# Kernel tuning notes

Measured on AMD Instinct MI355X. Metric: run time of the kernel, lower is better.

The kernel has to match this reference:

```python
import jax, jax.numpy as jnp
import numpy as np

HIDDEN = 4096
NUM_HEADS = 32
NUM_KV_HEADS = 8
HEAD_DIM = 128
EPS = 1e-6
ROPE_THETA = 1000000.0
T = 2048


def setup_inputs() -> dict:
    key = jax.random.key(0)
    k1, k2, k3, k4, k5 = jax.random.split(key, 5)
    q_size = NUM_HEADS * HEAD_DIM
    kv_size = NUM_KV_HEADS * HEAD_DIM
    return {
        "positions": jnp.arange(T, dtype=jnp.int32),
        "hidden_states": jax.random.normal(k1, (T, HIDDEN), dtype=jnp.float32),
        "w_qkv": jax.random.normal(k2, (HIDDEN, q_size + 2 * kv_size), dtype=jnp.float32) * 0.02,
        "w_o": jax.random.normal(k3, (q_size, HIDDEN), dtype=jnp.float32) * 0.02,
        "q_norm_w": jnp.ones((HEAD_DIM,), dtype=jnp.float32) + 0.01 * jax.random.normal(k4, (HEAD_DIM,), dtype=jnp.float32),
        "k_norm_w": jnp.ones((HEAD_DIM,), dtype=jnp.float32) + 0.01 * jax.random.normal(k5, (HEAD_DIM,), dtype=jnp.float32),
    }


def _rms_norm(x, w, eps=EPS):
    # x: [..., head_dim], normalize over last dim
    var = jnp.mean(jnp.square(x), axis=-1, keepdims=True)
    return x * jax.lax.rsqrt(var + eps) * w


def _apply_rope(x, positions):
    # neox-style rotate-half RoPE, rotary_dim == head_dim
    d = x.shape[-1]
    inv_freq = 1.0 / (ROPE_THETA ** (jnp.arange(0, d, 2, dtype=jnp.float32) / d))
    freqs = positions.astype(jnp.float32)[:, None] * inv_freq[None, :]  # [T, d/2]
    cos = jnp.cos(freqs)[:, None, :]  # [T, 1, d/2]
    sin = jnp.sin(freqs)[:, None, :]
    x1, x2 = jnp.split(x, 2, axis=-1)
    return jnp.concatenate([x1 * cos - x2 * sin, x2 * cos + x1 * sin], axis=-1)


def reference(positions, hidden_states, w_qkv, w_o, q_norm_w, k_norm_w):
    num_tokens = hidden_states.shape[0]
    q_size = NUM_HEADS * HEAD_DIM
    kv_size = NUM_KV_HEADS * HEAD_DIM
    group = NUM_HEADS // NUM_KV_HEADS

    qkv = hidden_states @ w_qkv  # [T, q+2kv]
    q = qkv[:, :q_size].reshape(num_tokens, NUM_HEADS, HEAD_DIM)
    k = qkv[:, q_size:q_size + kv_size].reshape(num_tokens, NUM_KV_HEADS, HEAD_DIM)
    v = qkv[:, q_size + kv_size:].reshape(num_tokens, NUM_KV_HEADS, HEAD_DIM)

    q = _rms_norm(q, q_norm_w)
    k = _rms_norm(k, k_norm_w)
    q = _apply_rope(q, positions)
    k = _apply_rope(k, positions)

    scale = HEAD_DIM ** -0.5
    # GQA: group query heads over shared kv heads
    qg = q.reshape(num_tokens, NUM_KV_HEADS, group, HEAD_DIM)
    scores = jnp.einsum("tkgd,skd->kgts", qg * scale, k)  # [KH, G, T, S]
    causal = positions[:, None] >= positions[None, :]  # [T, S]
    scores = jnp.where(causal[None, None, :, :], scores, jnp.finfo(scores.dtype).min)
    probs = jax.nn.softmax(scores, axis=-1)
    out = jnp.einsum("kgts,skd->tkgd", probs, v)  # [T, KH, G, D]
    out = out.reshape(num_tokens, q_size)
    return out @ w_o
```

## Files before the change

kernel.cpp:

```cpp
#include <hip/hip_runtime.h>
#include <cstdint>
#include <cstddef>

#define T_TOK 2048
#define HID   4096
#define NQH   32
#define NKVH  8
#define HD    128
#define QKV_N 6144

typedef __bf16 bf16x8 __attribute__((ext_vector_type(8)));
typedef __bf16 bf16x4 __attribute__((ext_vector_type(4)));
typedef float  f32x4  __attribute__((ext_vector_type(4)));
typedef float  f32x16 __attribute__((ext_vector_type(16)));

#define AS1 __attribute__((address_space(1)))
#define AS3 __attribute__((address_space(3)))

__device__ __forceinline__ void gll16(const void* g, void* l) {
  __builtin_amdgcn_global_load_lds((const AS1 void*)g, (AS3 void*)l, 16, 0, 0);
}

__global__ __launch_bounds__(256) void k_convert(const float* __restrict__ in,
                                                 __bf16* __restrict__ out, int n4) {
  int i = blockIdx.x * 256 + threadIdx.x;
  if (i >= n4) return;
  float4 v = ((const float4*)in)[i];
  bf16x4 o;
  o[0] = (__bf16)v.x; o[1] = (__bf16)v.y; o[2] = (__bf16)v.z; o[3] = (__bf16)v.w;
  ((bf16x4*)out)[i] = o;
}

__global__ __launch_bounds__(256) void k_transpose(const float* __restrict__ in,
                                                   __bf16* __restrict__ out,
                                                   int R, int C) {
  __shared__ float tile[64][33];
  const int tid = threadIdx.x;
  const int c0 = blockIdx.x * 32, r0 = blockIdx.y * 64;
  const int ty = tid >> 3, tx = tid & 7;
#pragma unroll
  for (int k = 0; k < 2; ++k) {
    float4 v = *(const float4*)&in[(size_t)(r0 + ty + k * 32) * C + c0 + tx * 4];
    tile[ty + k * 32][tx * 4 + 0] = v.x;
    tile[ty + k * 32][tx * 4 + 1] = v.y;
    tile[ty + k * 32][tx * 4 + 2] = v.z;
    tile[ty + k * 32][tx * 4 + 3] = v.w;
  }
  __syncthreads();
  const int c = tid >> 3, rq = tid & 7;
  bf16x8 o;
#pragma unroll
  for (int i = 0; i < 8; ++i) o[i] = (__bf16)tile[rq * 8 + i][c];
  *(bf16x8*)&out[(size_t)(c0 + c) * R + r0 + rq * 8] = o;
}

__global__ __launch_bounds__(256) void k_vtrans(const float* __restrict__ qkv,
                                                __bf16* __restrict__ vt) {
  __shared__ float tile[64][33];
  const int tid = threadIdx.x;
  const int kvh = blockIdx.z;
  const int d0 = blockIdx.x * 32;
  const int t0 = blockIdx.y * 64;
  const int ty = tid >> 3, tx = tid & 7;
#pragma unroll
  for (int k = 0; k < 2; ++k) {
    float4 v = *(const float4*)&qkv[(size_t)(t0 + ty + k * 32) * QKV_N + 5120 + kvh * 128 + d0 + tx * 4];
    tile[ty + k * 32][tx * 4 + 0] = v.x;
    tile[ty + k * 32][tx * 4 + 1] = v.y;
    tile[ty + k * 32][tx * 4 + 2] = v.z;
    tile[ty + k * 32][tx * 4 + 3] = v.w;
  }
  __syncthreads();
  const int d = tid >> 3, tq = tid & 7;
  bf16x8 o;
#pragma unroll
  for (int i = 0; i < 8; ++i) o[i] = (__bf16)tile[tq * 8 + i][d];
  *(bf16x8*)&vt[((size_t)kvh * 128 + d0 + d) * T_TOK + t0 + tq * 8] = o;
}

template <int NFR>
__global__ __launch_bounds__(512, 2) void k_gemm8(const __bf16* __restrict__ A,
                                                  const __bf16* __restrict__ Bt,
                                                  float* __restrict__ C,
                                                  int N, int K) {
  constexpr int BN   = 64 * NFR;
  constexpr int WN   = 16 * NFR;
  constexpr int NB   = NFR / 2;
  constexpr int NH   = NFR / 2;
  constexpr int BREG = BN * 64;
  constexpr int BUFSZ = 16384 + 2 * BREG;
  __shared__ alignas(16) char ldsb[2 * BUFSZ];
  const int tid = threadIdx.x;
  const int lane = tid & 63, w = tid >> 6;
  const int l16 = lane & 15, lg = lane >> 4;
  const int wm = w >> 2, wn = w & 3;

  const int x = blockIdx.x & 7, idx = blockIdx.x >> 3;
  const int bm = (x & 1) * 8 + (idx & 7);
  const int bn = (x >> 1) * 4 + (idx >> 3);

  const int rA = tid >> 2, pA = tid & 3;
  const __bf16* asrc = A + (size_t)(bm * 128 + rA) * K + ((pA ^ ((rA >> 1) & 3)) * 8);
  const __bf16* bsrc = Bt + (size_t)(bn * BN + rA) * K + ((pA ^ ((rA >> 1) & 3)) * 8);

#define RA_(buf, mk) (ldsb + (buf) * BUFSZ + (mk) * 8192)
#define RB_(buf, mk) (ldsb + (buf) * BUFSZ + 16384 + (mk) * BREG)
#define STG_A(buf, mk, kk) { gll16(asrc + (kk) + (mk) * 32, RA_(buf, mk) + w * 1024); }
#define STG_B(buf, mk, kk) { _Pragma("unroll") \
    for (int j = 0; j < NB; ++j) \
      gll16(bsrc + (size_t)j * 128 * K + (kk) + (mk) * 32, RB_(buf, mk) + j * 8192 + w * 1024); }
#define FRAG(base, row) (*(const bf16x8*)((base) + (row) * 64 + ((lg ^ (((row) >> 1) & 3)) << 4)))
#define WAITN() { if constexpr (NFR == 6) asm volatile("s_waitcnt vmcnt(4)" ::: "memory"); \
                  else                    asm volatile("s_waitcnt vmcnt(3)" ::: "memory"); }

  f32x4 acc[4][NFR] = {};
  const int nkt = K >> 6;

  STG_A(0, 0, 0); STG_B(0, 0, 0); STG_A(0, 1, 0); STG_B(0, 1, 0);

  for (int t = 0; t < nkt - 1; ++t) {
    const int cur = t & 1, nxt = cur ^ 1;
    const int kn = (t + 1) * 64;
    bf16x8 af[4], bf_[NH];

    STG_A(nxt, 0, kn);
    WAITN();
    __builtin_amdgcn_s_barrier();
    __builtin_amdgcn_sched_barrier(0);
#pragma unroll
    for (int i = 0; i < 4; ++i) af[i] = FRAG(RA_(cur, 0), wm * 64 + i * 16 + l16);
#pragma unroll
    for (int n = 0; n < NH; ++n) bf_[n] = FRAG(RB_(cur, 0), wn * WN + n * 16 + l16);
    __builtin_amdgcn_s_setprio(1);
#pragma unroll
    for (int i = 0; i < 4; ++i)
#pragma unroll
      for (int n = 0; n < NH; ++n)
        acc[i][n] = __builtin_amdgcn_mfma_f32_16x16x32_bf16(af[i], bf_[n], acc[i][n], 0, 0, 0);
    __builtin_amdgcn_s_setprio(0);
    __builtin_amdgcn_s_barrier();

#pragma unroll
    for (int n = 0; n < NH; ++n) bf_[n] = FRAG(RB_(cur, 0), wn * WN + (NH + n) * 16 + l16);
    STG_B(nxt, 0, kn);
    __builtin_amdgcn_s_barrier();
    __builtin_amdgcn_s_setprio(1);
#pragma unroll
    for (int i = 0; i < 4; ++i)
#pragma unroll
      for (int n = 0; n < NH; ++n)
        acc[i][NH + n] = __builtin_amdgcn_mfma_f32_16x16x32_bf16(af[i], bf_[n], acc[i][NH + n], 0, 0, 0);
    __builtin_amdgcn_s_setprio(0);
    __builtin_amdgcn_s_barrier();

    STG_A(nxt, 1, kn);
    WAITN();
    __builtin_amdgcn_s_barrier();
    __builtin_amdgcn_sched_barrier(0);
#pragma unroll
    for (int i = 0; i < 4; ++i) af[i] = FRAG(RA_(cur, 1), wm * 64 + i * 16 + l16);
#pragma unroll
    for (int n = 0; n < NH; ++n) bf_[n] = FRAG(RB_(cur, 1), wn * WN + n * 16 + l16);
    __builtin_amdgcn_s_setprio(1);
#pragma unroll
    for (int i = 0; i < 4; ++i)
#pragma unroll
      for (int n = 0; n < NH; ++n)
        acc[i][n] = __builtin_amdgcn_mfma_f32_16x16x32_bf16(af[i], bf_[n], acc[i][n], 0, 0, 0);
    __builtin_amdgcn_s_setprio(0);
    __builtin_amdgcn_s_barrier();

#pragma unroll
    for (int n = 0; n < NH; ++n) bf_[n] = FRAG(RB_(cur, 1), wn * WN + (NH + n) * 16 + l16);
    STG_B(nxt, 1, kn);
    __builtin_amdgcn_s_barrier();
    __builtin_amdgcn_s_setprio(1);
#pragma unroll
    for (int i = 0; i < 4; ++i)
#pragma unroll
      for (int n = 0; n < NH; ++n)
        acc[i][NH + n] = __builtin_amdgcn_mfma_f32_16x16x32_bf16(af[i], bf_[n], acc[i][NH + n], 0, 0, 0);
    __builtin_amdgcn_s_setprio(0);
    __builtin_amdgcn_s_barrier();
  }

  asm volatile("s_waitcnt vmcnt(0)" ::: "memory");
  __builtin_amdgcn_s_barrier();
  __builtin_amdgcn_sched_barrier(0);
  {
    const int cur = (nkt - 1) & 1;
#pragma unroll
    for (int mk = 0; mk < 2; ++mk) {
      bf16x8 aa[4], bb[NFR];
#pragma unroll
      for (int i = 0; i < 4; ++i) aa[i] = FRAG(RA_(cur, mk), wm * 64 + i * 16 + l16);
#pragma unroll
      for (int n = 0; n < NFR; ++n) bb[n] = FRAG(RB_(cur, mk), wn * WN + n * 16 + l16);
#pragma unroll
      for (int i = 0; i < 4; ++i)
#pragma unroll
        for (int n = 0; n < NFR; ++n)
          acc[i][n] = __builtin_amdgcn_mfma_f32_16x16x32_bf16(aa[i], bb[n], acc[i][n], 0, 0, 0);
    }
  }
#undef RA_
#undef RB_
#undef STG_A
#undef STG_B
#undef FRAG
#undef WAITN

#pragma unroll
  for (int mi = 0; mi < 4; ++mi)
#pragma unroll
    for (int ni = 0; ni < NFR; ++ni) {
      int row = bm * 128 + wm * 64 + mi * 16 + lg * 4;
      int col = bn * BN + wn * WN + ni * 16 + l16;
#pragma unroll
      for (int r = 0; r < 4; ++r)
        C[(size_t)(row + r) * N + col] = acc[mi][ni][r];
    }
}

__global__ __launch_bounds__(256) void k_norm_rope(const float* __restrict__ qkv,
                                                   const int* __restrict__ pos,
                                                   const float* __restrict__ qw,
                                                   const float* __restrict__ kw,
                                                   __bf16* __restrict__ qo,
                                                   __bf16* __restrict__ ko) {
  const int t = blockIdx.x;
  const int w = threadIdx.x >> 6, i = threadIdx.x & 63;
  const float fr = (float)pos[t] * expf((float)i * -0.21586735246819178f);
  const float cs = cosf(fr), sn = sinf(fr);
  const float qwi1 = qw[i], qwi2 = qw[i + 64];
  const float kwi1 = kw[i], kwi2 = kw[i + 64];
  const float* base = qkv + (size_t)t * QKV_N;
#pragma unroll
  for (int s = 0; s < 10; ++s) {
    const int slot = w * 10 + s;
    const int off = (slot < 32) ? slot * 128 : 4096 + (slot - 32) * 128;
    float x1 = base[off + i], x2 = base[off + i + 64];
    float ss = x1 * x1 + x2 * x2;
#pragma unroll
    for (int m = 32; m >= 1; m >>= 1) ss += __shfl_xor(ss, m);
    float rinv = rsqrtf(ss * (1.0f / 128.0f) + 1e-6f);
    float n1, n2;
    if (slot < 32) { n1 = x1 * rinv * qwi1; n2 = x2 * rinv * qwi2; }
    else           { n1 = x1 * rinv * kwi1; n2 = x2 * rinv * kwi2; }
    float o1 = n1 * cs - n2 * sn;
    float o2 = n2 * cs + n1 * sn;
    if (slot < 32) {
      const float QSC = 0.08838834764831845f * 1.4426950408889634f;
      __bf16* o = qo + ((size_t)t * NQH + slot) * HD;
      o[i] = (__bf16)(o1 * QSC);
      o[i + 64] = (__bf16)(o2 * QSC);
    } else {
      __bf16* o = ko + ((size_t)t * NKVH + (slot - 32)) * HD;
      o[i] = (__bf16)o1;
      o[i + 64] = (__bf16)o2;
    }
  }
}

__global__ __launch_bounds__(256, 2) void k_attn(const __bf16* __restrict__ Q,
                                                 const __bf16* __restrict__ K,
                                                 const __bf16* __restrict__ Vt,
                                                 __bf16* __restrict__ O) {
  __shared__ alignas(16) __bf16 Ks[64 * 128];
  __shared__ alignas(16) __bf16 Vts[128 * 64];
  const int bid = blockIdx.x;
  const int kvh = bid & 7;
  const int qc  = bid >> 3;
  const int tid = threadIdx.x, lane = tid & 63, w = tid >> 6;
  const int l31 = lane & 31, hi = lane >> 5;
  const int h  = kvh * 4 + w;
  const int q0 = qc * 32;
  const int qrow = q0 + l31;
  char* Ksb = (char*)Ks;
  char* Vtb = (char*)Vts;

  bf16x8 qf[8];
  {
    const __bf16* qp = Q + ((size_t)qrow * NQH + h) * HD + hi * 8;
#pragma unroll
    for (int dc = 0; dc < 8; ++dc)
      qf[dc] = *(const bf16x8*)(qp + dc * 16);
  }

  size_t ksrc[4], vsrc[4];
#pragma unroll
  for (int j = 0; j < 4; ++j) {
    int kr = w * 16 + j * 4 + (lane >> 4);
    ksrc[j] = ((size_t)kr * NKVH + kvh) * HD + (size_t)(((lane & 15) ^ (kr & 15)) * 8);
    int vr = w * 32 + j * 8 + (lane >> 3);
    vsrc[j] = ((size_t)(kvh * HD + vr)) * T_TOK + (size_t)(((lane & 7) ^ (vr & 7)) * 8);
  }

  float m_run = -3.0e38f, l_run = 0.f;
  f32x16 ot[4] = {};

  const int ntiles = (qc >> 1) + 1;
  for (int tt = 0; tt < ntiles; ++tt) {
    const int s0 = tt * 64;
#pragma unroll
    for (int j = 0; j < 4; ++j) {
      gll16(K + (size_t)s0 * (NKVH * HD) + ksrc[j], Ksb + (w * 4 + j) * 1024);
      gll16(Vt + (size_t)s0 + vsrc[j], Vtb + (w * 4 + j) * 1024);
    }
    __syncthreads();

    f32x16 sac[2] = {};
#pragma unroll
    for (int hf = 0; hf < 2; ++hf) {
      int krow = hf * 32 + l31;
#pragma unroll
      for (int dc = 0; dc < 8; ++dc) {
        bf16x8 kf = *(const bf16x8*)(Ksb + krow * 256 + (((dc * 2 + hi) ^ (krow & 15)) * 16));
        sac[hf] = __builtin_amdgcn_mfma_f32_32x32x16_bf16(kf, qf[dc], sac[hf], 0, 0, 0);
      }
    }

    float pv[32];
    if (s0 + 64 > q0) {
#pragma unroll
      for (int hf = 0; hf < 2; ++hf)
#pragma unroll
        for (int r = 0; r < 16; ++r) {
          int kvg = s0 + hf * 32 + (r & 3) + ((r >> 2) * 8) + hi * 4;
          pv[hf * 16 + r] = (kvg > qrow) ? -3.0e38f : sac[hf][r];
        }
    } else {
#pragma unroll
      for (int hf = 0; hf < 2; ++hf)
#pragma unroll
        for (int r = 0; r < 16; ++r) pv[hf * 16 + r] = sac[hf][r];
    }
    float t16[16];
#pragma unroll
    for (int i = 0; i < 16; ++i) t16[i] = fmaxf(pv[i], pv[i + 16]);
#pragma unroll
    for (int i = 0; i < 8; ++i) t16[i] = fmaxf(t16[i], t16[i + 8]);
#pragma unroll
    for (int i = 0; i < 4; ++i) t16[i] = fmaxf(t16[i], t16[i + 4]);
    float mt = fmaxf(fmaxf(t16[0], t16[1]), fmaxf(t16[2], t16[3]));
    mt = fmaxf(mt, __shfl_xor(mt, 32));
    if (!__all(mt - m_run <= 10.0f)) {
      float m_new = fmaxf(m_run, mt);
      float corr = exp2f(m_run - m_new);
      l_run *= corr;
#pragma unroll
      for (int dt = 0; dt < 4; ++dt)
#pragma unroll
        for (int r = 0; r < 16; ++r) ot[dt][r] *= corr;
      m_run = m_new;
    }
#pragma unroll
    for (int i = 0; i < 32; ++i) pv[i] = exp2f(pv[i] - m_run);
#pragma unroll
    for (int i = 0; i < 16; ++i) t16[i] = pv[i] + pv[i + 16];
#pragma unroll
    for (int i = 0; i < 8; ++i) t16[i] += t16[i + 8];
#pragma unroll
    for (int i = 0; i < 4; ++i) t16[i] += t16[i + 4];
    float rs = (t16[0] + t16[1]) + (t16[2] + t16[3]);
    rs += __shfl_xor(rs, 32);
    l_run += rs;

    uint32_t wds[16];
#pragma unroll
    for (int i = 0; i < 16; ++i) {
      uint32_t r;
      asm("v_cvt_pk_bf16_f32 %0, %1, %2" : "=v"(r) : "v"(pv[2 * i]), "v"(pv[2 * i + 1]));
      wds[i] = r;
    }
#pragma unroll
    for (int c = 0; c < 4; ++c) {
      const int base = (c >> 1) * 8 + (c & 1) * 4;
      uint32_t sa = hi ? wds[base + 0] : wds[base + 2];
      uint32_t sb = hi ? wds[base + 1] : wds[base + 3];
      uint32_t ra = __shfl_xor(sa, 32);
      uint32_t rb = __shfl_xor(sb, 32);
      union { uint32_t u[4]; bf16x8 v; } pf;
      pf.u[0] = hi ? ra : wds[base + 0];
      pf.u[1] = hi ? rb : wds[base + 1];
      pf.u[2] = hi ? wds[base + 2] : ra;
      pf.u[3] = hi ? wds[base + 3] : rb;
#pragma unroll
      for (int dt = 0; dt < 4; ++dt) {
        int vrow = dt * 32 + l31;
        bf16x8 vf = *(const bf16x8*)(Vtb + vrow * 128 + (((c * 2 + hi) ^ (vrow & 7)) * 16));
        ot[dt] = __builtin_amdgcn_mfma_f32_32x32x16_bf16(vf, pf.v, ot[dt], 0, 0, 0);
      }
    }
    __syncthreads();
  }

  float inv = 1.0f / l_run;
  char* Ob = Ksb + w * 8192;
#pragma unroll
  for (int dt = 0; dt < 4; ++dt)
#pragma unroll
    for (int r = 0; r < 16; ++r) {
      int d = dt * 32 + (r & 3) + ((r >> 2) * 8) + hi * 4;
      *(__bf16*)(Ob + l31 * 256 + ((d * 2) ^ ((l31 & 7) << 4))) = (__bf16)(ot[dt][r] * inv);
    }
#pragma unroll
  for (int pass = 0; pass < 8; ++pass) {
    int q = pass * 4 + (lane >> 4);
    int ch = lane & 15;
    bf16x8 vvv = *(const bf16x8*)(Ob + q * 256 + ((ch ^ (q & 7)) * 16));
    *(bf16x8*)(O + ((size_t)(q0 + q) * NQH + h) * HD + ch * 8) = vvv;
  }
}

extern "C" void kernel_launch(void* const* d_in, const int* in_sizes, int n_in,
                              void* d_out, int out_size, void* d_ws, size_t ws_size,
                              hipStream_t stream) {
  const int*   positions = (const int*)d_in[0];
  const float* hidden    = (const float*)d_in[1];
  const float* w_qkv     = (const float*)d_in[2];
  const float* w_o       = (const float*)d_in[3];
  const float* q_norm    = (const float*)d_in[4];
  const float* k_norm    = (const float*)d_in[5];
  float* out = (float*)d_out;

  char* ws = (char*)d_ws;
  __bf16* wqkv_t   = (__bf16*)ws;
  __bf16* wo_t     = (__bf16*)(ws + 50331648);
  __bf16* hidden_b = (__bf16*)(ws + 83886080);
  float*  qkv      = (float*)(ws + 100663296);
  __bf16* qb  = (__bf16*)ws;
  __bf16* kb  = (__bf16*)(ws + 16777216);
  __bf16* vtb = (__bf16*)(ws + 20971520);
  __bf16* attn_o = hidden_b;

  k_convert<<<dim3((T_TOK * HID / 4 + 255) / 256), 256, 0, stream>>>(hidden, hidden_b, T_TOK * HID / 4);
  k_transpose<<<dim3(QKV_N / 32, HID / 64), 256, 0, stream>>>(w_qkv, wqkv_t, HID, QKV_N);
  k_transpose<<<dim3(HID / 32, HID / 64), 256, 0, stream>>>(w_o, wo_t, HID, HID);
  k_gemm8<6><<<dim3(256), 512, 0, stream>>>(hidden_b, wqkv_t, qkv, QKV_N, HID);
  k_norm_rope<<<dim3(T_TOK), 256, 0, stream>>>(qkv, positions, q_norm, k_norm, qb, kb);
  k_vtrans<<<dim3(4, T_TOK / 64, NKVH), 256, 0, stream>>>(qkv, vtb);
  k_attn<<<dim3(512), 256, 0, stream>>>(qb, kb, vtb, attn_o);
  k_gemm8<4><<<dim3(256), 512, 0, stream>>>(attn_o, wo_t, out, HID, HID);
}
```

Before: 319.0 us.

## Load GEMM A fragments directly from global into registers, bypassing LDS

The GEMM no longer stages the A tile through LDS. Each wave loads its A fragments straight from global memory into registers, double-buffered across k-tiles, while B still goes through LDS via global_load_lds. This removes the LDS traffic and barrier work for A and halves the LDS footprint. The cost is that A rows shared by the four waves along N are fetched redundantly from global/L2, register pressure rises, and the vmcnt waits are re-tuned, which could stall on global latency.

```diff
diff --git a/kernel.cpp b/kernel.cpp
--- a/kernel.cpp
+++ b/kernel.cpp
@@ -79,16 +79,15 @@
 }
 
 template <int NFR>
-__global__ __launch_bounds__(512, 2) void k_gemm8(const __bf16* __restrict__ A,
+__global__ __launch_bounds__(512, 2) void k_gemma(const __bf16* __restrict__ A,
                                                   const __bf16* __restrict__ Bt,
                                                   float* __restrict__ C,
                                                   int N, int K) {
   constexpr int BN   = 64 * NFR;
   constexpr int WN   = 16 * NFR;
   constexpr int NB   = NFR / 2;
-  constexpr int NH   = NFR / 2;
   constexpr int BREG = BN * 64;
-  constexpr int BUFSZ = 16384 + 2 * BREG;
+  constexpr int BUFSZ = 2 * BREG;
   __shared__ alignas(16) char ldsb[2 * BUFSZ];
   const int tid = threadIdx.x;
   const int lane = tid & 63, w = tid >> 6;
@@ -99,90 +98,63 @@
   const int bm = (x & 1) * 8 + (idx & 7);
   const int bn = (x >> 1) * 4 + (idx >> 3);
 
-  const int rA = tid >> 2, pA = tid & 3;
-  const __bf16* asrc = A + (size_t)(bm * 128 + rA) * K + ((pA ^ ((rA >> 1) & 3)) * 8);
-  const __bf16* bsrc = Bt + (size_t)(bn * BN + rA) * K + ((pA ^ ((rA >> 1) & 3)) * 8);
-
-#define RA_(buf, mk) (ldsb + (buf) * BUFSZ + (mk) * 8192)
-#define RB_(buf, mk) (ldsb + (buf) * BUFSZ + 16384 + (mk) * BREG)
-#define STG_A(buf, mk, kk) { gll16(asrc + (kk) + (mk) * 32, RA_(buf, mk) + w * 1024); }
+  const int rB = tid >> 2, pB = tid & 3;
+  const __bf16* bsrc = Bt + (size_t)(bn * BN + rB) * K + ((pB ^ ((rB >> 1) & 3)) * 8);
+  const __bf16* abase = A + (size_t)(bm * 128 + wm * 64 + l16) * K + lg * 8;
+
+#define RB_(buf, mk) (ldsb + (buf) * BUFSZ + (mk) * BREG)
 #define STG_B(buf, mk, kk) { _Pragma("unroll") \
     for (int j = 0; j < NB; ++j) \
       gll16(bsrc + (size_t)j * 128 * K + (kk) + (mk) * 32, RB_(buf, mk) + j * 8192 + w * 1024); }
 #define FRAG(base, row) (*(const bf16x8*)((base) + (row) * 64 + ((lg ^ (((row) >> 1) & 3)) << 4)))
-#define WAITN() { if constexpr (NFR == 6) asm volatile("s_waitcnt vmcnt(4)" ::: "memory"); \
-                  else                    asm volatile("s_waitcnt vmcnt(3)" ::: "memory"); }
+#define ALOAD(dst, kt2) { _Pragma("unroll") \
+    for (int mi = 0; mi < 4; ++mi) _Pragma("unroll") \
+      for (int mk = 0; mk < 2; ++mk) \
+        dst[mi][mk] = *(const bf16x8*)(abase + (size_t)mi * 16 * K + (kt2) * 64 + mk * 32); }
+#define WAITN() { if constexpr (NFR == 6) asm volatile("s_waitcnt vmcnt(14)" ::: "memory"); \
+                  else                    asm volatile("s_waitcnt vmcnt(12)" ::: "memory"); }
+
+#define TILE(t_, AFU, AFN) { \
+    const int cur_ = (t_) & 1, nxt_ = cur_ ^ 1; \
+    const int kn_ = ((t_) + 1) * 64; \
+    STG_B(nxt_, 0, kn_); \
+    WAITN(); \
+    __builtin_amdgcn_s_barrier(); \
+    __builtin_amdgcn_sched_barrier(0); \
+    ALOAD(AFN, (t_) + 1); \
+    { bf16x8 bf_[NFR]; \
+      _Pragma("unroll") for (int n = 0; n < NFR; ++n) bf_[n] = FRAG(RB_(cur_, 0), wn * WN + n * 16 + l16); \
+      __builtin_amdgcn_s_setprio(1); \
+      _Pragma("unroll") for (int i = 0; i < 4; ++i) \
+        _Pragma("unroll") for (int n = 0; n < NFR; ++n) \
+          acc[i][n] = __builtin_amdgcn_mfma_f32_16x16x32_bf16(AFU[i][0], bf_[n], acc[i][n], 0, 0, 0); \
+      __builtin_amdgcn_s_setprio(0); } \
+    STG_B(nxt_, 1, kn_); \
+    WAITN(); \
+    __builtin_amdgcn_s_barrier(); \
+    __builtin_amdgcn_sched_barrier(0); \
+    { bf16x8 bf_[NFR]; \
+      _Pragma("unroll") for (int n = 0; n < NFR; ++n) bf_[n] = FRAG(RB_(cur_, 1), wn * WN + n * 16 + l16); \
+      __builtin_amdgcn_s_setprio(1); \
+      _Pragma("unroll") for (int i = 0; i < 4; ++i) \
+        _Pragma("unroll") for (int n = 0; n < NFR; ++n) \
+          acc[i][n] = __builtin_amdgcn_mfma_f32_16x16x32_bf16(AFU[i][1], bf_[n], acc[i][n], 0, 0, 0); \
+      __builtin_amdgcn_s_setprio(0); } \
+  }
 
   f32x4 acc[4][NFR] = {};
+  bf16x8 afA[4][2], afB[4][2];
   const int nkt = K >> 6;
 
-  STG_A(0, 0, 0); STG_B(0, 0, 0); STG_A(0, 1, 0); STG_B(0, 1, 0);
-
-  for (int t = 0; t < nkt - 1; ++t) {
-    const int cur = t & 1, nxt = cur ^ 1;
-    const int kn = (t + 1) * 64;
-    bf16x8 af[4], bf_[NH];
-
-    STG_A(nxt, 0, kn);
-    WAITN();
-    __builtin_amdgcn_s_barrier();
-    __builtin_amdgcn_sched_barrier(0);
-#pragma unroll
-    for (int i = 0; i < 4; ++i) af[i] = FRAG(RA_(cur, 0), wm * 64 + i * 16 + l16);
-#pragma unroll
-    for (int n = 0; n < NH; ++n) bf_[n] = FRAG(RB_(cur, 0), wn * WN + n * 16 + l16);
-    __builtin_amdgcn_s_setprio(1);
-#pragma unroll
-    for (int i = 0; i < 4; ++i)
-#pragma unroll
-      for (int n = 0; n < NH; ++n)
-        acc[i][n] = __builtin_amdgcn_mfma_f32_16x16x32_bf16(af[i], bf_[n], acc[i][n], 0, 0, 0);
-    __builtin_amdgcn_s_setprio(0);
-    __builtin_amdgcn_s_barrier();
-
-#pragma unroll
-    for (int n = 0; n < NH; ++n) bf_[n] = FRAG(RB_(cur, 0), wn * WN + (NH + n) * 16 + l16);
-    STG_B(nxt, 0, kn);
-    __builtin_amdgcn_s_barrier();
-    __builtin_amdgcn_s_setprio(1);
-#pragma unroll
-    for (int i = 0; i < 4; ++i)
-#pragma unroll
-      for (int n = 0; n < NH; ++n)
-        acc[i][NH + n] = __builtin_amdgcn_mfma_f32_16x16x32_bf16(af[i], bf_[n], acc[i][NH + n], 0, 0, 0);
-    __builtin_amdgcn_s_setprio(0);
-    __builtin_amdgcn_s_barrier();
-
-    STG_A(nxt, 1, kn);
-    WAITN();
-    __builtin_amdgcn_s_barrier();
-    __builtin_amdgcn_sched_barrier(0);
-#pragma unroll
-    for (int i = 0; i < 4; ++i) af[i] = FRAG(RA_(cur, 1), wm * 64 + i * 16 + l16);
-#pragma unroll
-    for (int n = 0; n < NH; ++n) bf_[n] = FRAG(RB_(cur, 1), wn * WN + n * 16 + l16);
-    __builtin_amdgcn_s_setprio(1);
-#pragma unroll
-    for (int i = 0; i < 4; ++i)
-#pragma unroll
-      for (int n = 0; n < NH; ++n)
-        acc[i][n] = __builtin_amdgcn_mfma_f32_16x16x32_bf16(af[i], bf_[n], acc[i][n], 0, 0, 0);
-    __builtin_amdgcn_s_setprio(0);
-    __builtin_amdgcn_s_barrier();
-
-#pragma unroll
-    for (int n = 0; n < NH; ++n) bf_[n] = FRAG(RB_(cur, 1), wn * WN + (NH + n) * 16 + l16);
-    STG_B(nxt, 1, kn);
-    __builtin_amdgcn_s_barrier();
-    __builtin_amdgcn_s_setprio(1);
-#pragma unroll
-    for (int i = 0; i < 4; ++i)
-#pragma unroll
-      for (int n = 0; n < NH; ++n)
-        acc[i][NH + n] = __builtin_amdgcn_mfma_f32_16x16x32_bf16(af[i], bf_[n], acc[i][NH + n], 0, 0, 0);
-    __builtin_amdgcn_s_setprio(0);
-    __builtin_amdgcn_s_barrier();
-  }
+  STG_B(0, 0, 0); STG_B(0, 1, 0);
+  ALOAD(afA, 0);
+
+  int t = 0;
+  for (; t + 2 < nkt; t += 2) {
+    TILE(t, afA, afB);
+    TILE(t + 1, afB, afA);
+  }
+  TILE(t, afA, afB);
 
   asm volatile("s_waitcnt vmcnt(0)" ::: "memory");
   __builtin_amdgcn_s_barrier();
@@ -191,24 +163,22 @@
     const int cur = (nkt - 1) & 1;
 #pragma unroll
     for (int mk = 0; mk < 2; ++mk) {
-      bf16x8 aa[4], bb[NFR];
-#pragma unroll
-      for (int i = 0; i < 4; ++i) aa[i] = FRAG(RA_(cur, mk), wm * 64 + i * 16 + l16);
+      bf16x8 bb[NFR];
 #pragma unroll
       for (int n = 0; n < NFR; ++n) bb[n] = FRAG(RB_(cur, mk), wn * WN + n * 16 + l16);
 #pragma unroll
       for (int i = 0; i < 4; ++i)
 #pragma unroll
         for (int n = 0; n < NFR; ++n)
-          acc[i][n] = __builtin_amdgcn_mfma_f32_16x16x32_bf16(aa[i], bb[n], acc[i][n], 0, 0, 0);
-    }
-  }
-#undef RA_
+          acc[i][n] = __builtin_amdgcn_mfma_f32_16x16x32_bf16(afB[i][mk], bb[n], acc[i][n], 0, 0, 0);
+    }
+  }
 #undef RB_
-#undef STG_A
 #undef STG_B
 #undef FRAG
+#undef ALOAD
 #undef WAITN
+#undef TILE
 
 #pragma unroll
   for (int mi = 0; mi < 4; ++mi)
@@ -437,9 +407,9 @@
   k_convert<<<dim3((T_TOK * HID / 4 + 255) / 256), 256, 0, stream>>>(hidden, hidden_b, T_TOK * HID / 4);
   k_transpose<<<dim3(QKV_N / 32, HID / 64), 256, 0, stream>>>(w_qkv, wqkv_t, HID, QKV_N);
   k_transpose<<<dim3(HID / 32, HID / 64), 256, 0, stream>>>(w_o, wo_t, HID, HID);
-  k_gemm8<6><<<dim3(256), 512, 0, stream>>>(hidden_b, wqkv_t, qkv, QKV_N, HID);
+  k_gemma<6><<<dim3(256), 512, 0, stream>>>(hidden_b, wqkv_t, qkv, QKV_N, HID);
   k_norm_rope<<<dim3(T_TOK), 256, 0, stream>>>(qkv, positions, q_norm, k_norm, qb, kb);
   k_vtrans<<<dim3(4, T_TOK / 64, NKVH), 256, 0, stream>>>(qkv, vtb);
   k_attn<<<dim3(512), 256, 0, stream>>>(qb, kb, vtb, attn_o);
-  k_gemm8<4><<<dim3(256), 512, 0, stream>>>(attn_o, wo_t, out, HID, HID);
-}
+  k_gemma<4><<<dim3(256), 512, 0, stream>>>(attn_o, wo_t, out, HID, HID);
+}
```

New measurement: 486.1 us. 52.3% more time.

## Double-buffer K/V tiles in attention kernel with async prefetch and wave priority

Applied to the files above, without the earlier changes.

The attention kernel now holds two LDS buffers for K and transposed V tiles. It issues global_load_lds for the next tile before computing on the current one, waiting with an explicit vmcnt count and raw s_barrier instead of __syncthreads. It also raises wave priority around the MFMA loops with s_setprio. The goal is to hide global-to-LDS load latency behind the QK and PV matrix math. In exchange, LDS use doubles to 64KB per block, which may cut occupancy below the two blocks per CU requested by launch bounds, and correctness now depends on the hand-written waitcnt counts.

```diff
diff --git a/kernel.cpp b/kernel.cpp
--- a/kernel.cpp
+++ b/kernel.cpp
@@ -266,8 +266,7 @@
                                                  const __bf16* __restrict__ K,
                                                  const __bf16* __restrict__ Vt,
                                                  __bf16* __restrict__ O) {
-  __shared__ alignas(16) __bf16 Ks[64 * 128];
-  __shared__ alignas(16) __bf16 Vts[128 * 64];
+  __shared__ alignas(16) char lds[2][32768];
   const int bid = blockIdx.x;
   const int kvh = bid & 7;
   const int qc  = bid >> 3;
@@ -276,8 +275,6 @@
   const int h  = kvh * 4 + w;
   const int q0 = qc * 32;
   const int qrow = q0 + l31;
-  char* Ksb = (char*)Ks;
-  char* Vtb = (char*)Vts;
 
   bf16x8 qf[8];
   {
@@ -296,20 +293,34 @@
     vsrc[j] = ((size_t)(kvh * HD + vr)) * T_TOK + (size_t)(((lane & 7) ^ (vr & 7)) * 8);
   }
 
+#define STAGE(buf, s0_) { _Pragma("unroll") \
+    for (int j = 0; j < 4; ++j) { \
+      gll16(K + (size_t)(s0_) * (NKVH * HD) + ksrc[j], lds[buf] + (w * 4 + j) * 1024); \
+      gll16(Vt + (size_t)(s0_) + vsrc[j], lds[buf] + 16384 + (w * 4 + j) * 1024); \
+    } }
+
   float m_run = -3.0e38f, l_run = 0.f;
   f32x16 ot[4] = {};
 
   const int ntiles = (qc >> 1) + 1;
+  STAGE(0, 0);
+  int cur = 0;
+
   for (int tt = 0; tt < ntiles; ++tt) {
     const int s0 = tt * 64;
-#pragma unroll
-    for (int j = 0; j < 4; ++j) {
-      gll16(K + (size_t)s0 * (NKVH * HD) + ksrc[j], Ksb + (w * 4 + j) * 1024);
-      gll16(Vt + (size_t)s0 + vsrc[j], Vtb + (w * 4 + j) * 1024);
-    }
-    __syncthreads();
+    if (tt + 1 < ntiles) {
+      STAGE(cur ^ 1, s0 + 64);
+      asm volatile("s_waitcnt vmcnt(8)" ::: "memory");
+    } else {
+      asm volatile("s_waitcnt vmcnt(0)" ::: "memory");
+    }
+    __builtin_amdgcn_s_barrier();
+    __builtin_amdgcn_sched_barrier(0);
+    char* Ksb = &lds[cur][0];
+    char* Vtb = &lds[cur][16384];
 
     f32x16 sac[2] = {};
+    __builtin_amdgcn_s_setprio(1);
 #pragma unroll
     for (int hf = 0; hf < 2; ++hf) {
       int krow = hf * 32 + l31;
@@ -319,6 +330,7 @@
         sac[hf] = __builtin_amdgcn_mfma_f32_32x32x16_bf16(kf, qf[dc], sac[hf], 0, 0, 0);
       }
     }
+    __builtin_amdgcn_s_setprio(0);
 
     float pv[32];
     if (s0 + 64 > q0) {
@@ -385,18 +397,21 @@
       pf.u[1] = hi ? rb : wds[base + 1];
       pf.u[2] = hi ? wds[base + 2] : ra;
       pf.u[3] = hi ? wds[base + 3] : rb;
+      __builtin_amdgcn_s_setprio(1);
 #pragma unroll
       for (int dt = 0; dt < 4; ++dt) {
         int vrow = dt * 32 + l31;
         bf16x8 vf = *(const bf16x8*)(Vtb + vrow * 128 + (((c * 2 + hi) ^ (vrow & 7)) * 16));
         ot[dt] = __builtin_amdgcn_mfma_f32_32x32x16_bf16(vf, pf.v, ot[dt], 0, 0, 0);
       }
-    }
-    __syncthreads();
+      __builtin_amdgcn_s_setprio(0);
+    }
+    __builtin_amdgcn_s_barrier();
+    cur ^= 1;
   }
 
   float inv = 1.0f / l_run;
-  char* Ob = Ksb + w * 8192;
+  char* Ob = &lds[0][0] + w * 8192;
 #pragma unroll
   for (int dt = 0; dt < 4; ++dt)
 #pragma unroll
@@ -404,6 +419,7 @@
       int d = dt * 32 + (r & 3) + ((r >> 2) * 8) + hi * 4;
       *(__bf16*)(Ob + l31 * 256 + ((d * 2) ^ ((l31 & 7) << 4))) = (__bf16)(ot[dt][r] * inv);
     }
+  __builtin_amdgcn_s_barrier();
 #pragma unroll
   for (int pass = 0; pass < 8; ++pass) {
     int q = pass * 4 + (lane >> 4);
@@ -411,6 +427,7 @@
     bf16x8 vvv = *(const bf16x8*)(Ob + q * 256 + ((ch ^ (q & 7)) * 16));
     *(bf16x8*)(O + ((size_t)(q0 + q) * NQH + h) * HD + ch * 8) = vvv;
   }
+#undef STAGE
 }
 
 extern "C" void kernel_launch(void* const* d_in, const int* in_sizes, int n_in,
```

After: 321.9 us. No clear change (+0.9%).

## Store QKV projection in bf16 and widen transpose tiles to 64x64

Applied to the files above, without the earlier changes.

The QKV GEMM now writes its output as bf16 instead of fp32 through a templated output type, and the norm/RoPE and V-transpose kernels read bf16. This halves the intermediate QKV write and read traffic. Separately, the weight and V transpose kernels use 64x64 tiles with each thread writing two 8-element vectors, which halves the block count. The bf16 rounding of QKV before the RMS norm adds some precision loss.

```diff
diff --git a/kernel.cpp b/kernel.cpp
--- a/kernel.cpp
+++ b/kernel.cpp
@@ -34,54 +34,58 @@
 __global__ __launch_bounds__(256) void k_transpose(const float* __restrict__ in,
                                                    __bf16* __restrict__ out,
                                                    int R, int C) {
-  __shared__ float tile[64][33];
+  __shared__ float tile[64][65];
   const int tid = threadIdx.x;
-  const int c0 = blockIdx.x * 32, r0 = blockIdx.y * 64;
-  const int ty = tid >> 3, tx = tid & 7;
-#pragma unroll
-  for (int k = 0; k < 2; ++k) {
-    float4 v = *(const float4*)&in[(size_t)(r0 + ty + k * 32) * C + c0 + tx * 4];
-    tile[ty + k * 32][tx * 4 + 0] = v.x;
-    tile[ty + k * 32][tx * 4 + 1] = v.y;
-    tile[ty + k * 32][tx * 4 + 2] = v.z;
-    tile[ty + k * 32][tx * 4 + 3] = v.w;
+  const int c0 = blockIdx.x * 64, r0 = blockIdx.y * 64;
+  const int ty = tid >> 4, tx = tid & 15;
+#pragma unroll
+  for (int k = 0; k < 4; ++k) {
+    float4 v = *(const float4*)&in[(size_t)(r0 + ty + k * 16) * C + c0 + tx * 4];
+    tile[ty + k * 16][tx * 4 + 0] = v.x;
+    tile[ty + k * 16][tx * 4 + 1] = v.y;
+    tile[ty + k * 16][tx * 4 + 2] = v.z;
+    tile[ty + k * 16][tx * 4 + 3] = v.w;
   }
   __syncthreads();
-  const int c = tid >> 3, rq = tid & 7;
-  bf16x8 o;
-#pragma unroll
-  for (int i = 0; i < 8; ++i) o[i] = (__bf16)tile[rq * 8 + i][c];
-  *(bf16x8*)&out[(size_t)(c0 + c) * R + r0 + rq * 8] = o;
-}
-
-__global__ __launch_bounds__(256) void k_vtrans(const float* __restrict__ qkv,
+  const int c = tid >> 2, rq = tid & 3;
+#pragma unroll
+  for (int h = 0; h < 2; ++h) {
+    bf16x8 o;
+#pragma unroll
+    for (int i = 0; i < 8; ++i) o[i] = (__bf16)tile[rq * 16 + h * 8 + i][c];
+    *(bf16x8*)&out[(size_t)(c0 + c) * R + r0 + rq * 16 + h * 8] = o;
+  }
+}
+
+__global__ __launch_bounds__(256) void k_vtrans(const __bf16* __restrict__ qkv,
                                                 __bf16* __restrict__ vt) {
-  __shared__ float tile[64][33];
+  __shared__ float tile[64][65];
   const int tid = threadIdx.x;
   const int kvh = blockIdx.z;
-  const int d0 = blockIdx.x * 32;
+  const int d0 = blockIdx.x * 64;
   const int t0 = blockIdx.y * 64;
-  const int ty = tid >> 3, tx = tid & 7;
-#pragma unroll
-  for (int k = 0; k < 2; ++k) {
-    float4 v = *(const float4*)&qkv[(size_t)(t0 + ty + k * 32) * QKV_N + 5120 + kvh * 128 + d0 + tx * 4];
-    tile[ty + k * 32][tx * 4 + 0] = v.x;
-    tile[ty + k * 32][tx * 4 + 1] = v.y;
-    tile[ty + k * 32][tx * 4 + 2] = v.z;
-    tile[ty + k * 32][tx * 4 + 3] = v.w;
+  const int ty = tid >> 4, tx = tid & 15;
+#pragma unroll
+  for (int k = 0; k < 4; ++k) {
+    bf16x4 v = *(const bf16x4*)&qkv[(size_t)(t0 + ty + k * 16) * QKV_N + 5120 + kvh * 128 + d0 + tx * 4];
+#pragma unroll
+    for (int j = 0; j < 4; ++j) tile[ty + k * 16][tx * 4 + j] = (float)v[j];
   }
   __syncthreads();
-  const int d = tid >> 3, tq = tid & 7;
-  bf16x8 o;
-#pragma unroll
-  for (int i = 0; i < 8; ++i) o[i] = (__bf16)tile[tq * 8 + i][d];
-  *(bf16x8*)&vt[((size_t)kvh * 128 + d0 + d) * T_TOK + t0 + tq * 8] = o;
-}
-
-template <int NFR>
+  const int d = tid >> 2, tq = tid & 3;
+#pragma unroll
+  for (int h = 0; h < 2; ++h) {
+    bf16x8 o;
+#pragma unroll
+    for (int i = 0; i < 8; ++i) o[i] = (__bf16)tile[tq * 16 + h * 8 + i][d];
+    *(bf16x8*)&vt[((size_t)kvh * 128 + d0 + d) * T_TOK + t0 + tq * 16 + h * 8] = o;
+  }
+}
+
+template <int NFR, typename OUT>
 __global__ __launch_bounds__(512, 2) void k_gemm8(const __bf16* __restrict__ A,
                                                   const __bf16* __restrict__ Bt,
-                                                  float* __restrict__ C,
+                                                  OUT* __restrict__ C,
                                                   int N, int K) {
   constexpr int BN   = 64 * NFR;
   constexpr int WN   = 16 * NFR;
@@ -218,11 +222,11 @@
       int col = bn * BN + wn * WN + ni * 16 + l16;
 #pragma unroll
       for (int r = 0; r < 4; ++r)
-        C[(size_t)(row + r) * N + col] = acc[mi][ni][r];
-    }
-}
-
-__global__ __launch_bounds__(256) void k_norm_rope(const float* __restrict__ qkv,
+        C[(size_t)(row + r) * N + col] = (OUT)acc[mi][ni][r];
+    }
+}
+
+__global__ __launch_bounds__(256) void k_norm_rope(const __bf16* __restrict__ qkv,
                                                    const int* __restrict__ pos,
                                                    const float* __restrict__ qw,
                                                    const float* __restrict__ kw,
@@ -234,12 +238,12 @@
   const float cs = cosf(fr), sn = sinf(fr);
   const float qwi1 = qw[i], qwi2 = qw[i + 64];
   const float kwi1 = kw[i], kwi2 = kw[i + 64];
-  const float* base = qkv + (size_t)t * QKV_N;
+  const __bf16* base = qkv + (size_t)t * QKV_N;
 #pragma unroll
   for (int s = 0; s < 10; ++s) {
     const int slot = w * 10 + s;
     const int off = (slot < 32) ? slot * 128 : 4096 + (slot - 32) * 128;
-    float x1 = base[off + i], x2 = base[off + i + 64];
+    float x1 = (float)base[off + i], x2 = (float)base[off + i + 64];
     float ss = x1 * x1 + x2 * x2;
 #pragma unroll
     for (int m = 32; m >= 1; m >>= 1) ss += __shfl_xor(ss, m);
@@ -428,18 +432,18 @@
   __bf16* wqkv_t   = (__bf16*)ws;
   __bf16* wo_t     = (__bf16*)(ws + 50331648);
   __bf16* hidden_b = (__bf16*)(ws + 83886080);
-  float*  qkv      = (float*)(ws + 100663296);
+  __bf16* qkvb     = (__bf16*)(ws + 100663296);
   __bf16* qb  = (__bf16*)ws;
   __bf16* kb  = (__bf16*)(ws + 16777216);
   __bf16* vtb = (__bf16*)(ws + 20971520);
   __bf16* attn_o = hidden_b;
 
   k_convert<<<dim3((T_TOK * HID / 4 + 255) / 256), 256, 0, stream>>>(hidden, hidden_b, T_TOK * HID / 4);
-  k_transpose<<<dim3(QKV_N / 32, HID / 64), 256, 0, stream>>>(w_qkv, wqkv_t, HID, QKV_N);
-  k_transpose<<<dim3(HID / 32, HID / 64), 256, 0, stream>>>(w_o, wo_t, HID, HID);
-  k_gemm8<6><<<dim3(256), 512, 0, stream>>>(hidden_b, wqkv_t, qkv, QKV_N, HID);
-  k_norm_rope<<<dim3(T_TOK), 256, 0, stream>>>(qkv, positions, q_norm, k_norm, qb, kb);
-  k_vtrans<<<dim3(4, T_TOK / 64, NKVH), 256, 0, stream>>>(qkv, vtb);
+  k_transpose<<<dim3(QKV_N / 64, HID / 64), 256, 0, stream>>>(w_qkv, wqkv_t, HID, QKV_N);
+  k_transpose<<<dim3(HID / 64, HID / 64), 256, 0, stream>>>(w_o, wo_t, HID, HID);
+  k_gemm8<6, __bf16><<<dim3(256), 512, 0, stream>>>(hidden_b, wqkv_t, qkvb, QKV_N, HID);
+  k_norm_rope<<<dim3(T_TOK), 256, 0, stream>>>(qkvb, positions, q_norm, k_norm, qb, kb);
+  k_vtrans<<<dim3(2, T_TOK / 64, NKVH), 256, 0, stream>>>(qkvb, vtb);
   k_attn<<<dim3(512), 256, 0, stream>>>(qb, kb, vtb, attn_o);
-  k_gemm8<4><<<dim3(256), 512, 0, stream>>>(attn_o, wo_t, out, HID, HID);
-}
+  k_gemm8<4, float><<<dim3(256), 512, 0, stream>>>(attn_o, wo_t, out, HID, HID);
+}
```

Result: no change. 315.4 us (-1.1%).
